# Kernel tuning notes

Hardware: AMD Instinct MI355X
Metric: run time of the kernel (lower is better)

The kernel has to match this reference:

```python
import jax, jax.numpy as jnp
import numpy as np

N = 8192  # number of ReLU nodes; abstract matrices are (N+1)x(N+1)


def setup_inputs() -> dict:
    key = jax.random.key(0)
    k1, k2 = jax.random.split(key)
    a = jax.random.normal(k1, (N,), dtype=jnp.float32)
    b = jax.random.normal(k2, (N,), dtype=jnp.float32)
    lower = jnp.minimum(a, b)
    upper = jnp.maximum(a, b)
    # alphas initialized exactly as in the module: 1e-5 if u < -l else 1.0
    alphas = jnp.where(upper < -lower, jnp.float32(1e-5), jnp.float32(1.0))
    return {"lower": lower, "upper": upper, "alphas": alphas}


def reference(lower, upper, alphas):
    n = lower.shape[0]
    l, u = lower, upper
    active = (u > 0) & (l >= 0)      # identity relaxation
    unstable = (u > 0) & (l < 0)     # triangle relaxation; u <= 0 -> all zeros
    a = jnp.clip(alphas, 0.0, 1.0)
    denom = u - l
    lam = u / jnp.where(denom == 0, jnp.ones_like(denom), denom)

    diag_low = jnp.where(active, 1.0, jnp.where(unstable, a, 0.0))
    diag_up = jnp.where(active, 1.0, jnp.where(unstable, lam, 0.0))
    bias_up = jnp.where(unstable, -lam * l, 0.0)  # last-row bias of upper relaxation

    conc_low = jnp.where(active, l, jnp.where(unstable, a * l, 0.0))
    conc_up = jnp.where(u > 0, u, 0.0)

    idx = jnp.arange(n)
    A_low = (jnp.zeros((n + 1, n + 1), dtype=lower.dtype)
             .at[idx, idx].set(diag_low)
             .at[n, n].set(1.0))
    A_up = (jnp.zeros((n + 1, n + 1), dtype=lower.dtype)
            .at[idx, idx].set(diag_up)
            .at[n, :n].set(bias_up)
            .at[n, n].set(1.0))
    return conc_low, conc_up, A_low, A_up
```

## Files before the change

kernel.cpp:

```cpp
#include <hip/hip_runtime.h>
#include <stdint.h>


typedef float f32x4 __attribute__((ext_vector_type(4)));

struct NodeVals { float diag_low, diag_up, bias_up, conc_low, conc_up; };

__device__ __forceinline__ NodeVals node_vals(float l, float u, float a_raw) {
    NodeVals nv;
    float a = fminf(fmaxf(a_raw, 0.f), 1.f);
    bool active   = (u > 0.f) && (l >= 0.f);
    bool unstable = (u > 0.f) && (l < 0.f);
    float denom = u - l;
    float lam = u / ((denom == 0.f) ? 1.f : denom);
    nv.diag_low = active ? 1.f : (unstable ? a : 0.f);
    nv.diag_up  = active ? 1.f : (unstable ? lam : 0.f);
    nv.bias_up  = unstable ? (-lam * l) : 0.f;
    nv.conc_low = active ? l : (unstable ? (a * l) : 0.f);
    nv.conc_up  = (u > 0.f) ? u : 0.f;
    return nv;
}

template <uint32_t NP1>
__global__ __launch_bounds__(256) void fused_fill(
        const float* __restrict__ lower,
        const float* __restrict__ upper,
        const float* __restrict__ alphas,
        float* __restrict__ out) {
    constexpr uint32_t N    = NP1 - 1;
    constexpr size_t   NPSQ = (size_t)NP1 * NP1;
    constexpr size_t   CONC = 2 * (size_t)N;
    constexpr size_t   T    = CONC + 2 * NPSQ;
    constexpr size_t   C4   = T / 4;
    static_assert(CONC % 4 == 0, "conc region must be float4-aligned");
    static_assert(T % 4 == 2, "tail handling assumes 2 trailing elements");

    f32x4* __restrict__ out4 = (f32x4*)out;
    const size_t stride = (size_t)gridDim.x * blockDim.x;

    for (size_t j = (size_t)blockIdx.x * blockDim.x + threadIdx.x; j < C4; j += stride) {
        const size_t e0 = j * 4;
        f32x4 v = (f32x4){0.f, 0.f, 0.f, 0.f};

        if (e0 < CONC) {
            if (e0 < (size_t)N) {
                const f32x4 l4 = *(const f32x4*)(lower  + e0);
                const f32x4 u4 = *(const f32x4*)(upper  + e0);
                const f32x4 a4 = *(const f32x4*)(alphas + e0);
                v[0] = node_vals(l4[0], u4[0], a4[0]).conc_low;
                v[1] = node_vals(l4[1], u4[1], a4[1]).conc_low;
                v[2] = node_vals(l4[2], u4[2], a4[2]).conc_low;
                v[3] = node_vals(l4[3], u4[3], a4[3]).conc_low;
            } else {
                const f32x4 u4 = *(const f32x4*)(upper + (e0 - N));
                v[0] = (u4[0] > 0.f) ? u4[0] : 0.f;
                v[1] = (u4[1] > 0.f) ? u4[1] : 0.f;
                v[2] = (u4[2] > 0.f) ? u4[2] : 0.f;
                v[3] = (u4[3] > 0.f) ? u4[3] : 0.f;
            }
        } else {
            const size_t g = e0 - CONC;
            int      mat = (g >= NPSQ) ? 1 : 0;
            uint32_t h   = (uint32_t)(mat ? (g - NPSQ) : g);
            uint32_t r   = h / NP1;
            uint32_t c   = h - r * NP1;

            const bool slow = (c > (uint32_t)(NP1 - 4)) |
                              ((uint32_t)(r - c) <= 3u) |
                              ((mat != 0) & (r == N));
            if (slow) {
                int m_ = mat; uint32_t rr = r, cc = c;
                #pragma unroll
                for (int k = 0; k < 4; ++k) {
                    float val = 0.f;
                    if (rr == cc) {
                        if (rr == N) {
                            val = 1.f;
                        } else {
                            NodeVals nv = node_vals(lower[rr], upper[rr], alphas[rr]);
                            val = m_ ? nv.diag_up : nv.diag_low;
                        }
                    } else if (m_ && rr == N) {
                        NodeVals nv = node_vals(lower[cc], upper[cc], alphas[cc]);
                        val = nv.bias_up;
                    }
                    v[k] = val;
                    ++cc;
                    if (cc == NP1) { cc = 0; ++rr; if (rr == NP1) { rr = 0; m_ = 1; } }
                }
            }
        }
        __builtin_nontemporal_store(v, out4 + j);
    }

    if (blockIdx.x == 0 && threadIdx.x == 0) {
        NodeVals nv = node_vals(lower[N - 1], upper[N - 1], alphas[N - 1]);
        out[T - 2] = nv.bias_up;
        out[T - 1] = 1.f;
    }
}

__global__ void generic_fill(const float* __restrict__ lower,
                             const float* __restrict__ upper,
                             const float* __restrict__ alphas,
                             float* __restrict__ out, int n) {
    const uint32_t np1  = (uint32_t)n + 1;
    const size_t   npsq = (size_t)np1 * np1;
    const size_t   conc = 2 * (size_t)n;
    const size_t   T    = conc + 2 * npsq;
    const size_t stride = (size_t)gridDim.x * blockDim.x;
    for (size_t e = (size_t)blockIdx.x * blockDim.x + threadIdx.x; e < T; e += stride) {
        float val = 0.f;
        if (e < (size_t)n) {
            val = node_vals(lower[e], upper[e], alphas[e]).conc_low;
        } else if (e < conc) {
            size_t i = e - n;
            val = node_vals(lower[i], upper[i], alphas[i]).conc_up;
        } else {
            size_t g = e - conc;
            int mat = (g >= npsq) ? 1 : 0;
            size_t h = mat ? (g - npsq) : g;
            uint32_t r = (uint32_t)(h / np1);
            uint32_t c = (uint32_t)(h - (size_t)r * np1);
            if (r == c) {
                if (r == (uint32_t)n) val = 1.f;
                else {
                    NodeVals nv = node_vals(lower[r], upper[r], alphas[r]);
                    val = mat ? nv.diag_up : nv.diag_low;
                }
            } else if (mat && r == (uint32_t)n) {
                val = node_vals(lower[c], upper[c], alphas[c]).bias_up;
            }
        }
        out[e] = val;
    }
}

extern "C" void kernel_launch(void* const* d_in, const int* in_sizes, int n_in,
                              void* d_out, int out_size, void* d_ws, size_t ws_size,
                              hipStream_t stream) {
    const float* lower  = (const float*)d_in[0];
    const float* upper  = (const float*)d_in[1];
    const float* alphas = (const float*)d_in[2];
    float* out = (float*)d_out;
    const int n = in_sizes[0];

    if (n == 8192) {
        fused_fill<8193><<<4096, 256, 0, stream>>>(lower, upper, alphas, out);
    } else {
        generic_fill<<<2048, 256, 0, stream>>>(lower, upper, alphas, out, n);
    }
}
```

Baseline: 556.7 us.

## Write 64 contiguous bytes per thread with 32-bit indexing and plain stores

Each thread now handles a group of 16 floats written as four consecutive float4 stores, instead of one float4 per loop iteration. Index arithmetic moves from 64-bit to 32-bit, the nontemporal store builtin is replaced with ordinary stores, and the grid is halved to 2048 blocks. The aim is to cut per-element index and division overhead on this write-bound fill. The trade-off is that each lane's stores are now strided by 64 bytes, which may hurt coalescing, and dropping the nontemporal hint may add cache pollution.

```diff
diff --git a/kernel.cpp b/kernel.cpp
--- a/kernel.cpp
+++ b/kernel.cpp
@@ -27,76 +27,96 @@
         const float* __restrict__ upper,
         const float* __restrict__ alphas,
         float* __restrict__ out) {
-    constexpr uint32_t N    = NP1 - 1;
-    constexpr size_t   NPSQ = (size_t)NP1 * NP1;
-    constexpr size_t   CONC = 2 * (size_t)N;
-    constexpr size_t   T    = CONC + 2 * NPSQ;
-    constexpr size_t   C4   = T / 4;
-    static_assert(CONC % 4 == 0, "conc region must be float4-aligned");
-    static_assert(T % 4 == 2, "tail handling assumes 2 trailing elements");
+    constexpr uint32_t N     = NP1 - 1;
+    constexpr uint32_t NPSQ  = NP1 * NP1;
+    constexpr uint32_t CONC  = 2 * N;
+    constexpr uint32_t T     = CONC + 2 * NPSQ;
+    constexpr uint32_t G     = (T - 2) / 16;
+    static_assert(N % 16 == 0, "conc region must be group-aligned");
+    static_assert(CONC % 16 == 0, "conc region must be group-aligned");
+    static_assert(T % 16 == 2, "tail handling assumes 2 trailing elements");
 
     f32x4* __restrict__ out4 = (f32x4*)out;
-    const size_t stride = (size_t)gridDim.x * blockDim.x;
+    const uint32_t stride = gridDim.x * blockDim.x;
 
-    for (size_t j = (size_t)blockIdx.x * blockDim.x + threadIdx.x; j < C4; j += stride) {
-        const size_t e0 = j * 4;
-        f32x4 v = (f32x4){0.f, 0.f, 0.f, 0.f};
+    for (uint32_t j = blockIdx.x * blockDim.x + threadIdx.x; j < G; j += stride) {
+        const uint32_t e0 = j * 16u;
+        f32x4* dst = out4 + (size_t)j * 4;
 
         if (e0 < CONC) {
-            if (e0 < (size_t)N) {
-                const f32x4 l4 = *(const f32x4*)(lower  + e0);
-                const f32x4 u4 = *(const f32x4*)(upper  + e0);
-                const f32x4 a4 = *(const f32x4*)(alphas + e0);
-                v[0] = node_vals(l4[0], u4[0], a4[0]).conc_low;
-                v[1] = node_vals(l4[1], u4[1], a4[1]).conc_low;
-                v[2] = node_vals(l4[2], u4[2], a4[2]).conc_low;
-                v[3] = node_vals(l4[3], u4[3], a4[3]).conc_low;
+            if (e0 < N) {
+                #pragma unroll
+                for (int s = 0; s < 4; ++s) {
+                    const uint32_t b = e0 + 4u * s;
+                    const f32x4 l4 = *(const f32x4*)(lower  + b);
+                    const f32x4 u4 = *(const f32x4*)(upper  + b);
+                    const f32x4 a4 = *(const f32x4*)(alphas + b);
+                    f32x4 v;
+                    #pragma unroll
+                    for (int k = 0; k < 4; ++k)
+                        v[k] = node_vals(l4[k], u4[k], a4[k]).conc_low;
+                    dst[s] = v;
+                }
             } else {
-                const f32x4 u4 = *(const f32x4*)(upper + (e0 - N));
-                v[0] = (u4[0] > 0.f) ? u4[0] : 0.f;
-                v[1] = (u4[1] > 0.f) ? u4[1] : 0.f;
-                v[2] = (u4[2] > 0.f) ? u4[2] : 0.f;
-                v[3] = (u4[3] > 0.f) ? u4[3] : 0.f;
+                #pragma unroll
+                for (int s = 0; s < 4; ++s) {
+                    const uint32_t b = e0 - N + 4u * s;
+                    const f32x4 u4 = *(const f32x4*)(upper + b);
+                    f32x4 v;
+                    #pragma unroll
+                    for (int k = 0; k < 4; ++k)
+                        v[k] = (u4[k] > 0.f) ? u4[k] : 0.f;
+                    dst[s] = v;
+                }
             }
         } else {
-            const size_t g = e0 - CONC;
-            int      mat = (g >= NPSQ) ? 1 : 0;
-            uint32_t h   = (uint32_t)(mat ? (g - NPSQ) : g);
-            uint32_t r   = h / NP1;
-            uint32_t c   = h - r * NP1;
+            const uint32_t g   = e0 - CONC;
+            const uint32_t mat = (g >= NPSQ) ? 1u : 0u;
+            const uint32_t h   = mat ? (g - NPSQ) : g;
+            const uint32_t r   = h / NP1;
+            const uint32_t c   = h - r * NP1;
 
-            const bool slow = (c > (uint32_t)(NP1 - 4)) |
-                              ((uint32_t)(r - c) <= 3u) |
-                              ((mat != 0) & (r == N));
-            if (slow) {
-                int m_ = mat; uint32_t rr = r, cc = c;
+            const bool slow = ((r - c) < 16u) |
+                              (c > (uint32_t)(NP1 - 16)) |
+                              ((mat != 0u) & (r == N));
+            if (!slow) {
+                const f32x4 z = (f32x4){0.f, 0.f, 0.f, 0.f};
+                dst[0] = z; dst[1] = z; dst[2] = z; dst[3] = z;
+            } else {
                 #pragma unroll
-                for (int k = 0; k < 4; ++k) {
-                    float val = 0.f;
-                    if (rr == cc) {
-                        if (rr == N) {
-                            val = 1.f;
-                        } else {
-                            NodeVals nv = node_vals(lower[rr], upper[rr], alphas[rr]);
-                            val = m_ ? nv.diag_up : nv.diag_low;
+                for (int s = 0; s < 4; ++s) {
+                    f32x4 v;
+                    #pragma unroll
+                    for (int k = 0; k < 4; ++k) {
+                        const uint32_t gk = g + 4u * s + k;
+                        const uint32_t mk = (gk >= NPSQ) ? 1u : 0u;
+                        const uint32_t hk = mk ? (gk - NPSQ) : gk;
+                        const uint32_t rk = hk / NP1;
+                        const uint32_t ck = hk - rk * NP1;
+                        float val = 0.f;
+                        if (rk == ck) {
+                            if (rk == N) {
+                                val = 1.f;
+                            } else {
+                                NodeVals nv = node_vals(lower[rk], upper[rk], alphas[rk]);
+                                val = mk ? nv.diag_up : nv.diag_low;
+                            }
+                        } else if (mk && rk == N) {
+                            NodeVals nv = node_vals(lower[ck], upper[ck], alphas[ck]);
+                            val = nv.bias_up;
                         }
-                    } else if (m_ && rr == N) {
-                        NodeVals nv = node_vals(lower[cc], upper[cc], alphas[cc]);
-                        val = nv.bias_up;
+                        v[k] = val;
                     }
-                    v[k] = val;
-                    ++cc;
-                    if (cc == NP1) { cc = 0; ++rr; if (rr == NP1) { rr = 0; m_ = 1; } }
+                    dst[s] = v;
                 }
             }
         }
-        __builtin_nontemporal_store(v, out4 + j);
     }
 
     if (blockIdx.x == 0 && threadIdx.x == 0) {
         NodeVals nv = node_vals(lower[N - 1], upper[N - 1], alphas[N - 1]);
-        out[T - 2] = nv.bias_up;
-        out[T - 1] = 1.f;
+        out[(size_t)T - 2] = nv.bias_up;
+        out[(size_t)T - 1] = 1.f;
     }
 }
 
@@ -146,7 +166,7 @@
     const int n = in_sizes[0];
 
     if (n == 8192) {
-        fused_fill<8193><<<4096, 256, 0, stream>>>(lower, upper, alphas, out);
+        fused_fill<8193><<<2048, 256, 0, stream>>>(lower, upper, alphas, out);
     } else {
         generic_fill<<<2048, 256, 0, stream>>>(lower, upper, alphas, out, n);
     }
```

Result: slower. 588.1 us (+5.6%).
